# Performance work log

Measured on AMD Instinct MI355X. Metric: run time of the kernel, lower is better.

## Reference

```python
import jax, jax.numpy as jnp
import numpy as np

ALPHA = 0.2
NOISE_STD = 0.05
I, H, O, R, S, G = 3, 2048, 2, 2, 4, 7
B, T = 32, 512


def _proxies(wi, unitwi, m, n, unitm, unitn, wo, h0, unith0, bias, gb, uv, sup):
    # gb: (G,H) gaussian basis, uv: (1,H) unit vector, sup: (S,H) support masks
    def comb(p, up):  # p: (K,S,G), up: (K,S,1) -> (K,H)
        return jnp.sum((jnp.einsum('ksg,gh->ksh', p, gb) + up * uv) * sup, axis=1)

    wi_full = comb(wi, unitwi)                                          # (I,H)
    m_rec = comb(m, unitm).T                                            # (H,R)
    n_rec = comb(n, unitn).T                                            # (H,R)
    wo_full = jnp.sum(jnp.einsum('osg,gh->osh', wo, gb) * sup, axis=1).T  # (H,O)
    h0_full = jnp.sum((h0 @ gb) * sup, axis=0) + jnp.sum((unith0 * uv) * sup, axis=0)  # (H,)
    bias_full = jnp.sum((bias * uv) * sup, axis=0)                      # (H,)
    w_rec = m_rec @ n_rec.T                                             # (H,H)
    return wi_full, wo_full, w_rec, h0_full, bias_full


def setup_inputs() -> dict:
    key = jax.random.key(0)
    ks = jax.random.split(key, 16)
    sc = 1.0 / np.sqrt(G)
    sup = np.zeros((S, H), dtype=np.float32)
    l = H // S
    for i in range(S):
        sup[i, l * i:l * (i + 1)] = 1.0
    return {
        'input': jax.random.normal(ks[0], (B, T, I), jnp.float32),
        'noise': jax.random.normal(ks[1], (B, T, H), jnp.float32),
        'wi': jax.random.normal(ks[2], (I, S, G), jnp.float32) * sc,
        'unitwi': jax.random.normal(ks[3], (I, S, 1), jnp.float32) * sc,
        'm': jax.random.normal(ks[4], (R, S, G), jnp.float32) * sc,
        'n': jax.random.normal(ks[5], (R, S, G), jnp.float32) * sc,
        'unitm': jax.random.normal(ks[6], (R, S, 1), jnp.float32) * sc,
        'unitn': jax.random.normal(ks[7], (R, S, 1), jnp.float32) * sc,
        'wo': jax.random.normal(ks[8], (O, S, G), jnp.float32) * sc,
        'h0': jax.random.normal(ks[9], (S, G), jnp.float32) * sc,
        'unith0': jax.random.normal(ks[10], (S, 1), jnp.float32) * sc,
        'bias': jax.random.normal(ks[11], (S, 1), jnp.float32) * 0.01,
        'gaussian_basis': jax.random.normal(ks[12], (G, H), jnp.float32),
        'unit_vector': jnp.ones((1, H), jnp.float32),
        'supports': jnp.asarray(sup),
    }


def reference(input, noise, wi, unitwi, m, n, unitm, unitn, wo, h0, unith0, bias,
              gaussian_basis, unit_vector, supports):
    wi_full, wo_full, w_rec, h0_full, bias_full = _proxies(
        wi, unitwi, m, n, unitm, unitn, wo, h0, unith0, bias,
        gaussian_basis, unit_vector, supports)
    batch = input.shape[0]
    h0b = jnp.broadcast_to(h0_full, (batch, h0_full.shape[0]))  # (B,H)

    def step(h, xs):
        x_t, z_t = xs                       # (B,I), (B,H)
        r = jnp.tanh(h)
        h = h + bias_full + NOISE_STD * z_t + ALPHA * (-h + r @ w_rec.T + x_t @ wi_full)
        r = jnp.tanh(h)
        return h, (r @ wo_full, h)

    _, (out, traj) = jax.lax.scan(step, h0b,
                                  (jnp.swapaxes(input, 0, 1), jnp.swapaxes(noise, 0, 1)))
    return jnp.swapaxes(out, 0, 1), jnp.swapaxes(traj, 0, 1)  # (B,T,O), (B,T,H)
```

## Files before the change

### kernel.cpp

```cpp
#include <hip/hip_runtime.h>

typedef float v2f __attribute__((ext_vector_type(2)));

constexpr int I_N = 3, H_N = 2048, O_N = 2, S_N = 4, G_N = 7;
constexpr int B_N = 32, T_N = 512;
constexpr int TPB = 512;
constexpr int EPT = H_N / TPB;
constexpr float ALPHA_C = 0.2f;
constexpr float NSTD_C = 0.05f;
constexpr float TWO_LOG2E = 2.885390081777927f;

__device__ __forceinline__ float fast_tanh(float x) {
  float e = __builtin_amdgcn_exp2f(x * TWO_LOG2E);
  return fmaf(-2.0f, __builtin_amdgcn_rcpf(e + 1.0f), 1.0f);
}

#define DPP_ADD(x, ctrl, rmask)                                                \
  x += __int_as_float(__builtin_amdgcn_update_dpp(                             \
      0, __float_as_int(x), (ctrl), (rmask), 0xf, true))

__device__ __forceinline__ float wave_sum63(float x) {
  DPP_ADD(x, 0x111, 0xf);
  DPP_ADD(x, 0x112, 0xf);
  DPP_ADD(x, 0x114, 0xf);
  DPP_ADD(x, 0x118, 0xf);
  DPP_ADD(x, 0x142, 0xa);
  DPP_ADD(x, 0x143, 0xc);
  return x;
}

__device__ __forceinline__ float rfl(float v) {
  return __int_as_float(__builtin_amdgcn_readfirstlane(__float_as_int(v)));
}

__global__ __launch_bounds__(TPB) void rnn_fused(
    const float* __restrict__ input,
    const float* __restrict__ noise,
    const float* __restrict__ wi,
    const float* __restrict__ unitwi,
    const float* __restrict__ m_,
    const float* __restrict__ n_,
    const float* __restrict__ unitm,
    const float* __restrict__ unitn,
    const float* __restrict__ wo,
    const float* __restrict__ h0,
    const float* __restrict__ unith0,
    const float* __restrict__ bias,
    const float* __restrict__ gb,
    const float* __restrict__ uv,
    const float* __restrict__ sup,
    float* __restrict__ out,
    float* __restrict__ traj) {
  const int tid = threadIdx.x;
  const int lane = tid & 63;
  const int wave = tid >> 6;
  const int b = blockIdx.x;
  const int hbase = tid * EPT;
  const int s = hbase >> 9;

  __shared__ float4 parts[2][16];
  __shared__ float4 xs4[T_N];

  float cn0[EPT], cn1[EPT], cm0[EPT], cm1[EPT];
  float cw0[EPT], cw1[EPT], cw2[EPT];
  float co0[EPT], co1[EPT], cb[EPT], hh_[EPT], r[EPT];

  for (int e = 0; e < EPT; ++e) {
    const int hh = hbase + e;
    float gbh[G_N];
#pragma unroll
    for (int g = 0; g < G_N; ++g) gbh[g] = gb[g * H_N + hh];
    const float uvh = uv[hh];
    const float sv = sup[s * H_N + hh];

    auto comb = [&](const float* p, const float* up, int k) {
      float acc = up[k * S_N + s] * uvh;
#pragma unroll
      for (int g = 0; g < G_N; ++g)
        acc = fmaf(p[(k * S_N + s) * G_N + g], gbh[g], acc);
      return acc * sv;
    };
    auto combNoU = [&](const float* p, int k) {
      float acc = 0.0f;
#pragma unroll
      for (int g = 0; g < G_N; ++g)
        acc = fmaf(p[(k * S_N + s) * G_N + g], gbh[g], acc);
      return acc * sv;
    };

    cn0[e] = comb(n_, unitn, 0);
    cn1[e] = comb(n_, unitn, 1);
    cm0[e] = ALPHA_C * comb(m_, unitm, 0);
    cm1[e] = ALPHA_C * comb(m_, unitm, 1);
    cw0[e] = ALPHA_C * comb(wi, unitwi, 0);
    cw1[e] = ALPHA_C * comb(wi, unitwi, 1);
    cw2[e] = ALPHA_C * comb(wi, unitwi, 2);
    co0[e] = combNoU(wo, 0);
    co1[e] = combNoU(wo, 1);
    cb[e] = bias[s] * uvh * sv;
    hh_[e] = comb(h0, unith0, 0);
    r[e] = fast_tanh(hh_[e]);
  }

  v2f cnp[EPT], cop[EPT];
  v2f cm0p[2], cm1p[2], cw0p[2], cw1p[2], cw2p[2], cbp[2];
#pragma unroll
  for (int e = 0; e < EPT; ++e) {
    cnp[e] = (v2f){cn0[e], cn1[e]};
    cop[e] = (v2f){co0[e], co1[e]};
  }
#pragma unroll
  for (int p2 = 0; p2 < 2; ++p2) {
    cm0p[p2] = (v2f){cm0[2 * p2], cm0[2 * p2 + 1]};
    cm1p[p2] = (v2f){cm1[2 * p2], cm1[2 * p2 + 1]};
    cw0p[p2] = (v2f){cw0[2 * p2], cw0[2 * p2 + 1]};
    cw1p[p2] = (v2f){cw1[2 * p2], cw1[2 * p2 + 1]};
    cw2p[p2] = (v2f){cw2[2 * p2], cw2[2 * p2 + 1]};
    cbp[p2] = (v2f){cb[2 * p2], cb[2 * p2 + 1]};
  }
  v2f h01 = (v2f){hh_[0], hh_[1]};
  v2f h23 = (v2f){hh_[2], hh_[3]};

  const float* zp = noise + ((size_t)b * T_N) * H_N + hbase;
  const float* xp = input + ((size_t)b * T_N) * I_N;
  float* tp = traj + ((size_t)b * T_N) * H_N + hbase;
  float* op = out + ((size_t)b * T_N) * O_N;

  {
    const float* xq = xp + tid * I_N;
    xs4[tid] = make_float4(xq[0], xq[1], xq[2], 0.0f);
  }
  if (tid < 16) parts[tid >> 3][8 + (tid & 7)] = make_float4(0.f, 0.f, 0.f, 0.f);

  float4 z0 = *(const float4*)zp;
  float4 z1 = *(const float4*)(zp + H_N);

  __builtin_amdgcn_s_waitcnt(0xC07F);
  __builtin_amdgcn_s_barrier();
  __asm__ volatile("" ::: "memory");

  float4 xv = xs4[0];

  auto body = [&](int t, int pb) {
    const int tz = (t + 2 < T_N) ? t + 2 : T_N - 1;
    float4 zn = *(const float4*)(zp + (size_t)tz * H_N);
    const int tx = (t + 1 < T_N) ? t + 1 : T_N - 1;
    float4 xn = xs4[tx];

    v2f z01 = (v2f){z0.x, z0.y}, z23 = (v2f){z0.z, z0.w};
    v2f pre01 = cbp[0];
    pre01 += NSTD_C * z01;
    pre01 += xv.x * cw0p[0];
    pre01 += xv.y * cw1p[0];
    pre01 += xv.z * cw2p[0];
    v2f pre23 = cbp[1];
    pre23 += NSTD_C * z23;
    pre23 += xv.x * cw0p[1];
    pre23 += xv.y * cw1p[1];
    pre23 += xv.z * cw2p[1];

    v2f accA = (v2f){0.f, 0.f}, accO = (v2f){0.f, 0.f};
#pragma unroll
    for (int e = 0; e < EPT; ++e) {
      v2f rr = (v2f){r[e], r[e]};
      accA += rr * cnp[e];
      accO += rr * cop[e];
    }
    float pa0 = wave_sum63(accA.x);
    float pa1 = wave_sum63(accA.y);
    float po0 = wave_sum63(accO.x);
    float po1 = wave_sum63(accO.y);
    if (lane == 63) parts[pb][wave] = make_float4(pa0, pa1, po0, po1);

    __builtin_amdgcn_s_waitcnt(0xC07F);
    __builtin_amdgcn_s_barrier();
    __asm__ volatile("" ::: "memory");

    float4 v = parts[pb][lane & 15];
    DPP_ADD(v.x, 0x101, 0xf); DPP_ADD(v.x, 0x102, 0xf); DPP_ADD(v.x, 0x104, 0xf);
    DPP_ADD(v.y, 0x101, 0xf); DPP_ADD(v.y, 0x102, 0xf); DPP_ADD(v.y, 0x104, 0xf);
    DPP_ADD(v.z, 0x101, 0xf); DPP_ADD(v.z, 0x102, 0xf); DPP_ADD(v.z, 0x104, 0xf);
    DPP_ADD(v.w, 0x101, 0xf); DPP_ADD(v.w, 0x102, 0xf); DPP_ADD(v.w, 0x104, 0xf);
    const float a0 = rfl(v.x);
    const float a1 = rfl(v.y);
    const float o0 = rfl(v.z);
    const float o1 = rfl(v.w);

    if (tid == 0 && t > 0) ((float2*)op)[t - 1] = make_float2(o0, o1);

    h01 = 0.8f * h01 + pre01;
    h01 += a0 * cm0p[0];
    h01 += a1 * cm1p[0];
    h23 = 0.8f * h23 + pre23;
    h23 += a0 * cm0p[1];
    h23 += a1 * cm1p[1];

    *(float4*)(tp + (size_t)t * H_N) = make_float4(h01.x, h01.y, h23.x, h23.y);

    r[0] = fast_tanh(h01.x);
    r[1] = fast_tanh(h01.y);
    r[2] = fast_tanh(h23.x);
    r[3] = fast_tanh(h23.y);

    z0 = z1; z1 = zn; xv = xn;
  };

  for (int t = 0; t < T_N; t += 2) {
    body(t, 0);
    body(t + 1, 1);
  }

  {
    v2f accO = (v2f){0.f, 0.f};
#pragma unroll
    for (int e = 0; e < EPT; ++e) {
      v2f rr = (v2f){r[e], r[e]};
      accO += rr * cop[e];
    }
    float po0 = wave_sum63(accO.x);
    float po1 = wave_sum63(accO.y);
    if (lane == 63) parts[0][wave] = make_float4(0.f, 0.f, po0, po1);
    __builtin_amdgcn_s_waitcnt(0xC07F);
    __builtin_amdgcn_s_barrier();
    __asm__ volatile("" ::: "memory");
    if (tid == 0) {
      float o0 = 0.f, o1 = 0.f;
#pragma unroll
      for (int w = 0; w < 8; ++w) {
        float4 pv = parts[0][w];
        o0 += pv.z;
        o1 += pv.w;
      }
      ((float2*)op)[T_N - 1] = make_float2(o0, o1);
    }
  }
}

extern "C" void kernel_launch(void* const* d_in, const int* in_sizes, int n_in,
                              void* d_out, int out_size, void* d_ws, size_t ws_size,
                              hipStream_t stream) {
  const float* input  = (const float*)d_in[0];
  const float* noise  = (const float*)d_in[1];
  const float* wi     = (const float*)d_in[2];
  const float* unitwi = (const float*)d_in[3];
  const float* m_     = (const float*)d_in[4];
  const float* n_     = (const float*)d_in[5];
  const float* unitm  = (const float*)d_in[6];
  const float* unitn  = (const float*)d_in[7];
  const float* wo     = (const float*)d_in[8];
  const float* h0     = (const float*)d_in[9];
  const float* unith0 = (const float*)d_in[10];
  const float* bias   = (const float*)d_in[11];
  const float* gb     = (const float*)d_in[12];
  const float* uv     = (const float*)d_in[13];
  const float* sup    = (const float*)d_in[14];

  float* out  = (float*)d_out;
  float* traj = out + (size_t)B_N * T_N * O_N;

  rnn_fused<<<dim3(B_N), dim3(TPB), 0, stream>>>(
      input, noise, wi, unitwi, m_, n_, unitm, unitn, wo, h0, unith0, bias,
      gb, uv, sup, out, traj);
}
```

Measured before the change: 495.8 us.

## Move output projection out of recurrent loop into separate parallel kernel

Removes the per-step output projection (two extra wave reductions, LDS traffic and DPP adds) from the serial recurrence, so each step's critical path carries only the rank-2 recurrent reduction. The output is recomputed afterward by a massively parallel kernel that rereads traj and applies tanh and the wo projection, with wo precomputed into workspace. Noise prefetch distance also grows from two to four steps. This adds two kernel launches and one extra full read of traj (about 128 MB) from memory.

Result: faster. 439.4 us (-11.4%).

```diff
diff --git a/kernel.cpp b/kernel.cpp
--- a/kernel.cpp
+++ b/kernel.cpp
@@ -31,6 +31,63 @@
 
 __device__ __forceinline__ float rfl(float v) {
   return __int_as_float(__builtin_amdgcn_readfirstlane(__float_as_int(v)));
+}
+
+__global__ __launch_bounds__(256) void wo_precomp(
+    const float* __restrict__ wo, const float* __restrict__ gb,
+    const float* __restrict__ sup, float2* __restrict__ ws2) {
+  const int h = blockIdx.x * 256 + threadIdx.x;
+  const int s = h >> 9;
+  const float sv = sup[s * H_N + h];
+  float c0 = 0.f, c1 = 0.f;
+#pragma unroll
+  for (int g = 0; g < G_N; ++g) {
+    const float gv = gb[g * H_N + h];
+    c0 = fmaf(wo[(0 * S_N + s) * G_N + g], gv, c0);
+    c1 = fmaf(wo[(1 * S_N + s) * G_N + g], gv, c1);
+  }
+  ws2[h] = make_float2(c0 * sv, c1 * sv);
+}
+
+__global__ __launch_bounds__(256) void out_proj(
+    const float* __restrict__ traj, const float2* __restrict__ ws2,
+    float* __restrict__ out) {
+  const int blk = blockIdx.x;
+  const int tid = threadIdx.x;
+  const int lane = tid & 63;
+  const int wave = tid >> 6;
+  const int hb = tid * 8;
+
+  __shared__ float2 red[4];
+
+  const float* tp = traj + (size_t)blk * H_N + hb;
+  float4 t0 = *(const float4*)tp;
+  float4 t1 = *(const float4*)(tp + 4);
+  float2 c[8];
+#pragma unroll
+  for (int e = 0; e < 8; ++e) c[e] = ws2[hb + e];
+
+  float hv[8] = {t0.x, t0.y, t0.z, t0.w, t1.x, t1.y, t1.z, t1.w};
+  float p0 = 0.f, p1 = 0.f;
+#pragma unroll
+  for (int e = 0; e < 8; ++e) {
+    const float rv = fast_tanh(hv[e]);
+    p0 = fmaf(rv, c[e].x, p0);
+    p1 = fmaf(rv, c[e].y, p1);
+  }
+  p0 = wave_sum63(p0);
+  p1 = wave_sum63(p1);
+  if (lane == 63) red[wave] = make_float2(p0, p1);
+  __syncthreads();
+  if (tid == 0) {
+    float o0 = 0.f, o1 = 0.f;
+#pragma unroll
+    for (int w = 0; w < 4; ++w) {
+      o0 += red[w].x;
+      o1 += red[w].y;
+    }
+    ((float2*)out)[blk] = make_float2(o0, o1);
+  }
 }
 
 __global__ __launch_bounds__(TPB) void rnn_fused(
@@ -42,14 +99,12 @@
     const float* __restrict__ n_,
     const float* __restrict__ unitm,
     const float* __restrict__ unitn,
-    const float* __restrict__ wo,
     const float* __restrict__ h0,
     const float* __restrict__ unith0,
     const float* __restrict__ bias,
     const float* __restrict__ gb,
     const float* __restrict__ uv,
     const float* __restrict__ sup,
-    float* __restrict__ out,
     float* __restrict__ traj) {
   const int tid = threadIdx.x;
   const int lane = tid & 63;
@@ -58,12 +113,12 @@
   const int hbase = tid * EPT;
   const int s = hbase >> 9;
 
-  __shared__ float4 parts[2][16];
+  __shared__ float2 parts[2][16];
   __shared__ float4 xs4[T_N];
 
   float cn0[EPT], cn1[EPT], cm0[EPT], cm1[EPT];
   float cw0[EPT], cw1[EPT], cw2[EPT];
-  float co0[EPT], co1[EPT], cb[EPT], hh_[EPT], r[EPT];
+  float cb[EPT], hh_[EPT], r[EPT];
 
   for (int e = 0; e < EPT; ++e) {
     const int hh = hbase + e;
@@ -75,13 +130,6 @@
 
     auto comb = [&](const float* p, const float* up, int k) {
       float acc = up[k * S_N + s] * uvh;
-#pragma unroll
-      for (int g = 0; g < G_N; ++g)
-        acc = fmaf(p[(k * S_N + s) * G_N + g], gbh[g], acc);
-      return acc * sv;
-    };
-    auto combNoU = [&](const float* p, int k) {
-      float acc = 0.0f;
 #pragma unroll
       for (int g = 0; g < G_N; ++g)
         acc = fmaf(p[(k * S_N + s) * G_N + g], gbh[g], acc);
@@ -95,20 +143,15 @@
     cw0[e] = ALPHA_C * comb(wi, unitwi, 0);
     cw1[e] = ALPHA_C * comb(wi, unitwi, 1);
     cw2[e] = ALPHA_C * comb(wi, unitwi, 2);
-    co0[e] = combNoU(wo, 0);
-    co1[e] = combNoU(wo, 1);
     cb[e] = bias[s] * uvh * sv;
     hh_[e] = comb(h0, unith0, 0);
     r[e] = fast_tanh(hh_[e]);
   }
 
-  v2f cnp[EPT], cop[EPT];
+  v2f cnp[EPT];
   v2f cm0p[2], cm1p[2], cw0p[2], cw1p[2], cw2p[2], cbp[2];
 #pragma unroll
-  for (int e = 0; e < EPT; ++e) {
-    cnp[e] = (v2f){cn0[e], cn1[e]};
-    cop[e] = (v2f){co0[e], co1[e]};
-  }
+  for (int e = 0; e < EPT; ++e) cnp[e] = (v2f){cn0[e], cn1[e]};
 #pragma unroll
   for (int p2 = 0; p2 < 2; ++p2) {
     cm0p[p2] = (v2f){cm0[2 * p2], cm0[2 * p2 + 1]};
@@ -124,16 +167,17 @@
   const float* zp = noise + ((size_t)b * T_N) * H_N + hbase;
   const float* xp = input + ((size_t)b * T_N) * I_N;
   float* tp = traj + ((size_t)b * T_N) * H_N + hbase;
-  float* op = out + ((size_t)b * T_N) * O_N;
 
   {
     const float* xq = xp + tid * I_N;
     xs4[tid] = make_float4(xq[0], xq[1], xq[2], 0.0f);
   }
-  if (tid < 16) parts[tid >> 3][8 + (tid & 7)] = make_float4(0.f, 0.f, 0.f, 0.f);
-
-  float4 z0 = *(const float4*)zp;
-  float4 z1 = *(const float4*)(zp + H_N);
+  if (tid < 16) parts[tid >> 3][8 + (tid & 7)] = make_float2(0.f, 0.f);
+
+  float4 zr0 = *(const float4*)zp;
+  float4 zr1 = *(const float4*)(zp + H_N);
+  float4 zr2 = *(const float4*)(zp + 2 * (size_t)H_N);
+  float4 zr3 = *(const float4*)(zp + 3 * (size_t)H_N);
 
   __builtin_amdgcn_s_waitcnt(0xC07F);
   __builtin_amdgcn_s_barrier();
@@ -141,8 +185,9 @@
 
   float4 xv = xs4[0];
 
-  auto body = [&](int t, int pb) {
-    const int tz = (t + 2 < T_N) ? t + 2 : T_N - 1;
+  auto body = [&](int t, int pb, float4& zslot) {
+    const float4 z0 = zslot;
+    const int tz = (t + 4 < T_N) ? t + 4 : T_N - 1;
     float4 zn = *(const float4*)(zp + (size_t)tz * H_N);
     const int tx = (t + 1 < T_N) ? t + 1 : T_N - 1;
     float4 xn = xs4[tx];
@@ -159,34 +204,25 @@
     pre23 += xv.y * cw1p[1];
     pre23 += xv.z * cw2p[1];
 
-    v2f accA = (v2f){0.f, 0.f}, accO = (v2f){0.f, 0.f};
+    v2f accA = (v2f){0.f, 0.f};
 #pragma unroll
     for (int e = 0; e < EPT; ++e) {
       v2f rr = (v2f){r[e], r[e]};
       accA += rr * cnp[e];
-      accO += rr * cop[e];
     }
     float pa0 = wave_sum63(accA.x);
     float pa1 = wave_sum63(accA.y);
-    float po0 = wave_sum63(accO.x);
-    float po1 = wave_sum63(accO.y);
-    if (lane == 63) parts[pb][wave] = make_float4(pa0, pa1, po0, po1);
+    if (lane == 63) parts[pb][wave] = make_float2(pa0, pa1);
 
     __builtin_amdgcn_s_waitcnt(0xC07F);
     __builtin_amdgcn_s_barrier();
     __asm__ volatile("" ::: "memory");
 
-    float4 v = parts[pb][lane & 15];
+    float2 v = parts[pb][lane & 15];
     DPP_ADD(v.x, 0x101, 0xf); DPP_ADD(v.x, 0x102, 0xf); DPP_ADD(v.x, 0x104, 0xf);
     DPP_ADD(v.y, 0x101, 0xf); DPP_ADD(v.y, 0x102, 0xf); DPP_ADD(v.y, 0x104, 0xf);
-    DPP_ADD(v.z, 0x101, 0xf); DPP_ADD(v.z, 0x102, 0xf); DPP_ADD(v.z, 0x104, 0xf);
-    DPP_ADD(v.w, 0x101, 0xf); DPP_ADD(v.w, 0x102, 0xf); DPP_ADD(v.w, 0x104, 0xf);
     const float a0 = rfl(v.x);
     const float a1 = rfl(v.y);
-    const float o0 = rfl(v.z);
-    const float o1 = rfl(v.w);
-
-    if (tid == 0 && t > 0) ((float2*)op)[t - 1] = make_float2(o0, o1);
 
     h01 = 0.8f * h01 + pre01;
     h01 += a0 * cm0p[0];
@@ -202,37 +238,15 @@
     r[2] = fast_tanh(h23.x);
     r[3] = fast_tanh(h23.y);
 
-    z0 = z1; z1 = zn; xv = xn;
+    zslot = zn;
+    xv = xn;
   };
 
-  for (int t = 0; t < T_N; t += 2) {
-    body(t, 0);
-    body(t + 1, 1);
-  }
-
-  {
-    v2f accO = (v2f){0.f, 0.f};
-#pragma unroll
-    for (int e = 0; e < EPT; ++e) {
-      v2f rr = (v2f){r[e], r[e]};
-      accO += rr * cop[e];
-    }
-    float po0 = wave_sum63(accO.x);
-    float po1 = wave_sum63(accO.y);
-    if (lane == 63) parts[0][wave] = make_float4(0.f, 0.f, po0, po1);
-    __builtin_amdgcn_s_waitcnt(0xC07F);
-    __builtin_amdgcn_s_barrier();
-    __asm__ volatile("" ::: "memory");
-    if (tid == 0) {
-      float o0 = 0.f, o1 = 0.f;
-#pragma unroll
-      for (int w = 0; w < 8; ++w) {
-        float4 pv = parts[0][w];
-        o0 += pv.z;
-        o1 += pv.w;
-      }
-      ((float2*)op)[T_N - 1] = make_float2(o0, o1);
-    }
+  for (int t = 0; t < T_N; t += 4) {
+    body(t, 0, zr0);
+    body(t + 1, 1, zr1);
+    body(t + 2, 0, zr2);
+    body(t + 3, 1, zr3);
   }
 }
 
@@ -257,8 +271,11 @@
 
   float* out  = (float*)d_out;
   float* traj = out + (size_t)B_N * T_N * O_N;
-
+  float2* ws2 = (float2*)d_ws;
+
+  wo_precomp<<<dim3(H_N / 256), dim3(256), 0, stream>>>(wo, gb, sup, ws2);
   rnn_fused<<<dim3(B_N), dim3(TPB), 0, stream>>>(
-      input, noise, wi, unitwi, m_, n_, unitm, unitn, wo, h0, unith0, bias,
-      gb, uv, sup, out, traj);
-}
+      input, noise, wi, unitwi, m_, n_, unitm, unitn, h0, unith0, bias,
+      gb, uv, sup, traj);
+  out_proj<<<dim3(B_N * T_N), dim3(256), 0, stream>>>(traj, ws2, out);
+}
```
